# Kernel tuning notes

Hardware: AMD Instinct MI355X
Metric: run time of the kernel (lower is better)

Reference implementation:

```python
import jax, jax.numpy as jnp
import numpy as np

N, E = 20000, 320000
IN_F, EF, H, C = 2, 1, 128, 2
BN_S = 1.0 / float(np.sqrt(1.0 + 1e-5))  # eval-mode BatchNorm1d with running mean 0, var 1


def _gated_gcn_conv(h, e, src, dst, p, act, residual):
    # DGL GatedGCNConv: e' = C e + D h_src + E h_dst;
    # h' = A h + sum_{in-edges} sigmoid(e') * B h_src / (sum sigmoid(e') + 1e-6)
    Aw, Ab, Bw, Bb, Cw, Cb, Dw, Db, Ew, Eb, bhg, bhb, beg, beb = p
    h_in, e_in = h, e
    Ah = h @ Aw + Ab
    Bh = h @ Bw + Bb
    Dh = h @ Dw + Db
    Eh = h @ Ew + Eb
    e2 = e @ Cw + Cb + Dh[src] + Eh[dst]          # [E, H]
    sig = jax.nn.sigmoid(e2)
    num = jax.ops.segment_sum(sig * Bh[src], dst, num_segments=N)  # [N, H]
    den = jax.ops.segment_sum(sig, dst, num_segments=N)            # [N, H]
    h2 = Ah + num / (den + 1e-6)
    # BatchNorm (eval): (x - 0)/sqrt(1 + eps) * gamma + beta
    h2 = bhg * (h2 * BN_S) + bhb
    e2 = beg * (e2 * BN_S) + beb
    h2, e2 = act(h2), act(e2)
    if residual:
        h2 = h2 + h_in
        e2 = e2 + e_in
    return h2, e2


def _forward(node_feats, edge_feats, src, dst, P):
    (a0_w, a0_b, b0_w, b0_b, c0_w, c0_b, d0_w, d0_b, e0_w, e0_b,
     bnh0_g, bnh0_b, bne0_g, bne0_b,
     aL_w, aL_b, bL_w, bL_b, cL_w, cL_b, dL_w, dL_b, eL_w, eL_b,
     bnhL_g, bnhL_b, bneL_g, bneL_b,
     mlp_w1, mlp_b1, mlp_w2, mlp_b2) = P
    h, e = node_feats, edge_feats
    # layer 0: elu inside conv, residual off (2->128, 1->128)
    p0 = (a0_w, a0_b, b0_w, b0_b, c0_w, c0_b, d0_w, d0_b, e0_w, e0_b,
          bnh0_g, bnh0_b, bne0_g, bne0_b)
    h, e = _gated_gcn_conv(h, e, src, dst, p0, jax.nn.elu, residual=False)
    h = jax.nn.leaky_relu(h)
    e = jax.nn.leaky_relu(e)
    # layers 1..2: leaky_relu inside conv, residual on (128->128)
    for l in range(2):
        pl = (aL_w[l], aL_b[l], bL_w[l], bL_b[l], cL_w[l], cL_b[l],
              dL_w[l], dL_b[l], eL_w[l], eL_b[l],
              bnhL_g[l], bnhL_b[l], bneL_g[l], bneL_b[l])
        h, e = _gated_gcn_conv(h, e, src, dst, pl, jax.nn.leaky_relu, residual=True)
        h = jax.nn.leaky_relu(h)
        e = jax.nn.leaky_relu(e)
    # edge classifier: gather endpoints, concat with edge feats, MLP
    edge_repr = jnp.concatenate([h[src], h[dst], e], axis=1)  # [E, 3H]
    hid = jax.nn.relu(edge_repr @ mlp_w1 + mlp_b1)
    return hid @ mlp_w2 + mlp_b2                               # [E, C]


PARAM_NAMES = ["a0_w", "a0_b", "b0_w", "b0_b", "c0_w", "c0_b", "d0_w", "d0_b",
               "e0_w", "e0_b", "bnh0_g", "bnh0_b", "bne0_g", "bne0_b",
               "aL_w", "aL_b", "bL_w", "bL_b", "cL_w", "cL_b", "dL_w", "dL_b",
               "eL_w", "eL_b", "bnhL_g", "bnhL_b", "bneL_g", "bneL_b",
               "mlp_w1", "mlp_b1", "mlp_w2", "mlp_b2"]


def setup_inputs() -> dict:
    key = jax.random.key(0)
    ks = iter(jax.random.split(key, 64))
    nrm = lambda shp: jax.random.normal(next(ks), shp, dtype=jnp.float32) * 0.05
    inp = {}
    inp["node_feats"] = jax.random.normal(next(ks), (N, IN_F), dtype=jnp.float32)
    inp["edge_feats"] = jax.random.normal(next(ks), (E, EF), dtype=jnp.float32)
    inp["src"] = jax.random.randint(next(ks), (E,), 0, N, dtype=jnp.int32)
    inp["dst"] = jax.random.randint(next(ks), (E,), 0, N, dtype=jnp.int32)
    # layer 0 linears (A,B,D,E: in->H; C: edge->H), biases zero-init like common practice
    for nm, din in [("a0", IN_F), ("b0", IN_F), ("c0", EF), ("d0", IN_F), ("e0", IN_F)]:
        inp[nm + "_w"] = nrm((din, H))
        inp[nm + "_b"] = nrm((H,))
    inp["bnh0_g"] = jnp.ones((H,), jnp.float32)
    inp["bnh0_b"] = jnp.zeros((H,), jnp.float32)
    inp["bne0_g"] = jnp.ones((H,), jnp.float32)
    inp["bne0_b"] = jnp.zeros((H,), jnp.float32)
    # layers 1..2 stacked
    for nm in ["aL", "bL", "cL", "dL", "eL"]:
        inp[nm + "_w"] = nrm((2, H, H))
        inp[nm + "_b"] = nrm((2, H))
    inp["bnhL_g"] = jnp.ones((2, H), jnp.float32)
    inp["bnhL_b"] = jnp.zeros((2, H), jnp.float32)
    inp["bneL_g"] = jnp.ones((2, H), jnp.float32)
    inp["bneL_b"] = jnp.zeros((2, H), jnp.float32)
    # edge MLP
    inp["mlp_w1"] = nrm((3 * H, H))
    inp["mlp_b1"] = nrm((H,))
    inp["mlp_w2"] = nrm((H, C))
    inp["mlp_b2"] = nrm((C,))
    return inp


def reference(node_feats, edge_feats, src, dst,
              a0_w, a0_b, b0_w, b0_b, c0_w, c0_b, d0_w, d0_b, e0_w, e0_b,
              bnh0_g, bnh0_b, bne0_g, bne0_b,
              aL_w, aL_b, bL_w, bL_b, cL_w, cL_b, dL_w, dL_b, eL_w, eL_b,
              bnhL_g, bnhL_b, bneL_g, bneL_b,
              mlp_w1, mlp_b1, mlp_w2, mlp_b2):
    P = (a0_w, a0_b, b0_w, b0_b, c0_w, c0_b, d0_w, d0_b, e0_w, e0_b,
         bnh0_g, bnh0_b, bne0_g, bne0_b,
         aL_w, aL_b, bL_w, bL_b, cL_w, cL_b, dL_w, dL_b, eL_w, eL_b,
         bnhL_g, bnhL_b, bneL_g, bneL_b,
         mlp_w1, mlp_b1, mlp_w2, mlp_b2)
    return _forward(node_feats, edge_feats, src, dst, P)
```

## Files before the change

### kernel.cpp

```cpp
#include <hip/hip_runtime.h>
#include <hip/hip_bf16.h>
#include <math.h>

#define NN 20000
#define NE 320000
#define H 128
#define NH (NN * H)

typedef short bf16x8 __attribute__((ext_vector_type(8)));
typedef float f32x4 __attribute__((ext_vector_type(4)));
typedef unsigned short u16x8 __attribute__((ext_vector_type(8)));

__device__ __forceinline__ float lrelu(float x) { return x > 0.f ? x : 0.01f * x; }
__device__ __forceinline__ float eluf(float x)  { return x > 0.f ? x : expm1f(x); }
__device__ __forceinline__ float sigf(float x)  { return 1.f / (1.f + __expf(-x)); }
__device__ __forceinline__ unsigned short f2b(float x) {
    __hip_bfloat16 h = __float2bfloat16(x);
    return *reinterpret_cast<unsigned short*>(&h);
}
__device__ __forceinline__ float b2f(unsigned short u) {
    __hip_bfloat16 h = *reinterpret_cast<__hip_bfloat16*>(&u);
    return __bfloat162float(h);
}
#define BN_S 0.99999500003749973f

struct PackPtrs { const float* w[13]; };
__global__ __launch_bounds__(256) void k_pack(PackPtrs p, unsigned short* __restrict__ dst) {
    int gid = blockIdx.x * 256 + threadIdx.x;
    int m = gid >> 11;
    int r = gid & 2047;
    int t = r >> 8, kk = (r >> 6) & 3, lane = r & 63;
    const float* W = p.w[m];
    int col = t * 16 + (lane & 15);
    int krow = kk * 32 + (lane >> 4) * 8;
    unsigned short* o = dst + (size_t)m * 16384 + (size_t)r * 8;
#pragma unroll
    for (int j = 0; j < 8; ++j) o[j] = f2b(W[(krow + j) * H + col]);
}

__global__ __launch_bounds__(256) void k_deg(const int* __restrict__ dst, int* __restrict__ deg) {
    int e = blockIdx.x * 256 + threadIdx.x;
    if (e < NE) atomicAdd(&deg[dst[e]], 1);
}

__global__ __launch_bounds__(256) void k_scan(const int* __restrict__ deg,
                                              int* __restrict__ off, int* __restrict__ cursor) {
    __shared__ int sums[256];
    const int t = threadIdx.x;
    const int per = (NN + 255) / 256;
    const int base = t * per;
    int s = 0;
    for (int i = 0; i < per; ++i) { int idx = base + i; if (idx < NN) s += deg[idx]; }
    sums[t] = s;
    __syncthreads();
    for (int d = 1; d < 256; d <<= 1) {
        int v = (t >= d) ? sums[t - d] : 0;
        __syncthreads();
        sums[t] += v;
        __syncthreads();
    }
    int run = (t == 0) ? 0 : sums[t - 1];
    for (int i = 0; i < per; ++i) {
        int idx = base + i;
        if (idx < NN) { off[idx] = run; cursor[idx] = run; run += deg[idx]; }
    }
}

__global__ __launch_bounds__(256) void k_fill(const int* __restrict__ dst,
                                              int* __restrict__ cursor, int* __restrict__ csr) {
    int e = blockIdx.x * 256 + threadIdx.x;
    if (e < NE) {
        int pos = atomicAdd(&cursor[dst[e]], 1);
        csr[pos] = e;
    }
}

__global__ __launch_bounds__(256) void k_seqs(const int* __restrict__ csr,
                                              const int* __restrict__ src,
                                              const int* __restrict__ dst,
                                              const float* __restrict__ ef,
                                              int* __restrict__ srcseq,
                                              int* __restrict__ dstseq,
                                              float* __restrict__ efseq) {
    int pos = blockIdx.x * 256 + threadIdx.x;
    if (pos < NE) {
        int eid = csr[pos];
        srcseq[pos] = src[eid];
        dstseq[pos] = dst[eid];
        efseq[pos]  = ef[eid];
    }
}

__global__ __launch_bounds__(256) void k_nodelin0(
        const float* __restrict__ nf,
        const float* __restrict__ wa, const float* __restrict__ ba,
        const float* __restrict__ wb, const float* __restrict__ bb,
        const float* __restrict__ wd, const float* __restrict__ bd,
        const float* __restrict__ we, const float* __restrict__ be,
        float* __restrict__ lin0, unsigned short* __restrict__ linB,
        unsigned short* __restrict__ linD, unsigned short* __restrict__ linE) {
    int idx = blockIdx.x * 256 + threadIdx.x;
    int n = idx >> 7, c = idx & 127;
    float x0 = nf[n * 2], x1 = nf[n * 2 + 1];
    lin0[idx] = fmaf(x0, wa[c], fmaf(x1, wa[128 + c], ba[c]));
    linB[idx] = f2b(fmaf(x0, wb[c], fmaf(x1, wb[128 + c], bb[c])));
    linD[idx] = f2b(fmaf(x0, wd[c], fmaf(x1, wd[128 + c], bd[c])));
    linE[idx] = f2b(fmaf(x0, we[c], fmaf(x1, we[128 + c], be[c])));
}

__global__ __launch_bounds__(256) void k_edge0(
        const float* __restrict__ efseq,
        const float* __restrict__ cw, const float* __restrict__ cb,
        const int* __restrict__ srcseq, const int* __restrict__ dstseq,
        const unsigned short* __restrict__ linD, const unsigned short* __restrict__ linE,
        const float* __restrict__ g, const float* __restrict__ bt,
        unsigned short* __restrict__ ebuf) {
    const int tid = threadIdx.x;
    const int pos = blockIdx.x * 8 + (tid >> 5);
    const int c0 = (tid & 31) * 4;
    const int s = srcseq[pos], d = dstseq[pos];
    const float ev = efseq[pos];
    const float4 cw4 = *(const float4*)(cw + c0);
    const float4 cb4 = *(const float4*)(cb + c0);
    const ushort4 Dh = *(const ushort4*)(linD + (size_t)s * H + c0);
    const ushort4 Eh = *(const ushort4*)(linE + (size_t)d * H + c0);
    const float4 g4  = *(const float4*)(g + c0);
    const float4 bt4 = *(const float4*)(bt + c0);
    float e2[4] = { fmaf(ev, cw4.x, cb4.x) + b2f(Dh.x) + b2f(Eh.x),
                    fmaf(ev, cw4.y, cb4.y) + b2f(Dh.y) + b2f(Eh.y),
                    fmaf(ev, cw4.z, cb4.z) + b2f(Dh.z) + b2f(Eh.z),
                    fmaf(ev, cw4.w, cb4.w) + b2f(Dh.w) + b2f(Eh.w) };
    const float gg[4] = { g4.x, g4.y, g4.z, g4.w };
    const float bb[4] = { bt4.x, bt4.y, bt4.z, bt4.w };
    ushort4 u;
    u.x = f2b(lrelu(eluf(fmaf(gg[0], e2[0] * BN_S, bb[0]))));
    u.y = f2b(lrelu(eluf(fmaf(gg[1], e2[1] * BN_S, bb[1]))));
    u.z = f2b(lrelu(eluf(fmaf(gg[2], e2[2] * BN_S, bb[2]))));
    u.w = f2b(lrelu(eluf(fmaf(gg[3], e2[3] * BN_S, bb[3]))));
    *(ushort4*)(ebuf + (size_t)pos * H + c0) = u;
}

__global__ __launch_bounds__(256) void k_agg0(
        const int* __restrict__ off, const int* __restrict__ deg,
        const int* __restrict__ srcseq, const float* __restrict__ efseq,
        const float* __restrict__ cw, const float* __restrict__ cb,
        const float* __restrict__ lin0, const unsigned short* __restrict__ linB,
        const unsigned short* __restrict__ linD, const unsigned short* __restrict__ linE,
        const float* __restrict__ g, const float* __restrict__ bt,
        float* __restrict__ hout, unsigned short* __restrict__ hbout) {
    const int tid = threadIdx.x;
    const int n = blockIdx.x * 2 + (tid >> 7);
    const int c = tid & 127;
    const int base = off[n], dg = deg[n];
    float num = 0.f, den = 0.f;
    const float Ehn = b2f(linE[(size_t)n * H + c]);
    const float cwc = cw[c], cbc = cb[c];
    int i = 0;
    for (; i + 4 <= dg; i += 4) {
        int s0 = srcseq[base + i],     s1 = srcseq[base + i + 1];
        int s2 = srcseq[base + i + 2], s3 = srcseq[base + i + 3];
        float x0 = fmaf(efseq[base + i],     cwc, cbc) + b2f(linD[(size_t)s0 * H + c]) + Ehn;
        float x1 = fmaf(efseq[base + i + 1], cwc, cbc) + b2f(linD[(size_t)s1 * H + c]) + Ehn;
        float x2 = fmaf(efseq[base + i + 2], cwc, cbc) + b2f(linD[(size_t)s2 * H + c]) + Ehn;
        float x3 = fmaf(efseq[base + i + 3], cwc, cbc) + b2f(linD[(size_t)s3 * H + c]) + Ehn;
        float g0 = sigf(x0), g1 = sigf(x1), g2 = sigf(x2), g3 = sigf(x3);
        num = fmaf(g0, b2f(linB[(size_t)s0 * H + c]), num); den += g0;
        num = fmaf(g1, b2f(linB[(size_t)s1 * H + c]), num); den += g1;
        num = fmaf(g2, b2f(linB[(size_t)s2 * H + c]), num); den += g2;
        num = fmaf(g3, b2f(linB[(size_t)s3 * H + c]), num); den += g3;
    }
    for (; i < dg; ++i) {
        int sa = srcseq[base + i];
        float xa = fmaf(efseq[base + i], cwc, cbc) + b2f(linD[(size_t)sa * H + c]) + Ehn;
        float ga = sigf(xa);
        num = fmaf(ga, b2f(linB[(size_t)sa * H + c]), num); den += ga;
    }
    float h2 = lin0[(size_t)n * H + c] + num / (den + 1e-6f);
    h2 = fmaf(g[c], h2 * BN_S, bt[c]);
    h2 = eluf(h2);
    float r = lrelu(h2);
    hout[(size_t)n * H + c] = r;
    hbout[(size_t)n * H + c] = f2b(r);
}

__global__ __launch_bounds__(256) void k_agg(
        const int* __restrict__ off, const int* __restrict__ deg,
        const int* __restrict__ srcseq,
        const unsigned short* __restrict__ e2seq,
        const float* __restrict__ lin0, const unsigned short* __restrict__ linB,
        const float* __restrict__ g, const float* __restrict__ bt,
        const float* __restrict__ hin, float* __restrict__ hout,
        unsigned short* __restrict__ hbout) {
    const int tid = threadIdx.x;
    const int n = blockIdx.x * 2 + (tid >> 7);
    const int c = tid & 127;
    const int base = off[n], dg = deg[n];
    float num = 0.f, den = 0.f;
    int i = 0;
    for (; i + 4 <= dg; i += 4) {
        int s0 = srcseq[base + i],     s1 = srcseq[base + i + 1];
        int s2 = srcseq[base + i + 2], s3 = srcseq[base + i + 3];
        float x0 = b2f(e2seq[(size_t)(base + i) * H + c]);
        float x1 = b2f(e2seq[(size_t)(base + i + 1) * H + c]);
        float x2 = b2f(e2seq[(size_t)(base + i + 2) * H + c]);
        float x3 = b2f(e2seq[(size_t)(base + i + 3) * H + c]);
        float g0 = sigf(x0), g1 = sigf(x1), g2 = sigf(x2), g3 = sigf(x3);
        num = fmaf(g0, b2f(linB[(size_t)s0 * H + c]), num); den += g0;
        num = fmaf(g1, b2f(linB[(size_t)s1 * H + c]), num); den += g1;
        num = fmaf(g2, b2f(linB[(size_t)s2 * H + c]), num); den += g2;
        num = fmaf(g3, b2f(linB[(size_t)s3 * H + c]), num); den += g3;
    }
    for (; i < dg; ++i) {
        int sa = srcseq[base + i];
        float xa = b2f(e2seq[(size_t)(base + i) * H + c]);
        float ga = sigf(xa);
        num = fmaf(ga, b2f(linB[(size_t)sa * H + c]), num); den += ga;
    }
    float h2 = lin0[(size_t)n * H + c] + num / (den + 1e-6f);
    h2 = fmaf(g[c], h2 * BN_S, bt[c]);
    h2 = lrelu(h2);
    h2 += hin[(size_t)n * H + c];
    float r = lrelu(h2);
    hout[(size_t)n * H + c] = r;
    hbout[(size_t)n * H + c] = f2b(r);
}

__global__ __launch_bounds__(256) void k_nodegemm(
        const unsigned short* __restrict__ hb,
        const unsigned short* __restrict__ wpack,
        const float* __restrict__ ba, const float* __restrict__ bb,
        const float* __restrict__ bd, const float* __restrict__ be,
        float* __restrict__ lin0, unsigned short* __restrict__ linB,
        unsigned short* __restrict__ linD, unsigned short* __restrict__ linE) {
    __shared__ __align__(16) unsigned short AT[64][136];
    const int tid = threadIdx.x;
    const int nbase = blockIdx.x * 64;
    const int which = blockIdx.y;
    const unsigned short* Wp = wpack + (size_t)which * 16384;
    const float* B = which == 0 ? ba : which == 1 ? bb : which == 2 ? bd : be;
#pragma unroll
    for (int rep = 0; rep < 4; ++rep) {
        int flat = (rep * 256 + tid) * 8;
        int r = flat >> 7, k0 = flat & 127;
        int n = nbase + r;
        u16x8 v = {};
        if (n < NN) v = *(const u16x8*)(hb + (size_t)n * H + k0);
        *(u16x8*)(&AT[r][k0]) = v;
    }
    __syncthreads();
    const int lane = tid & 63, wave = tid >> 6;
    const int lrow = lane & 15, quad = lane >> 4;
    f32x4 acc[8] = {};
#pragma unroll
    for (int kk = 0; kk < 4; ++kk) {
        bf16x8 af = *(const bf16x8*)(&AT[wave * 16 + lrow][kk * 32 + quad * 8]);
#pragma unroll
        for (int t = 0; t < 8; ++t) {
            bf16x8 bfv = *(const bf16x8*)(Wp + ((t * 4 + kk) * 64 + lane) * 8);
            acc[t] = __builtin_amdgcn_mfma_f32_16x16x32_bf16(af, bfv, acc[t], 0, 0, 0);
        }
    }
    unsigned short* linX = which == 1 ? linB : which == 2 ? linD : linE;
#pragma unroll
    for (int t = 0; t < 8; ++t) {
        int col = t * 16 + lrow;
        float bv = B[col];
#pragma unroll
        for (int reg = 0; reg < 4; ++reg) {
            int n = nbase + wave * 16 + quad * 4 + reg;
            if (n < NN) {
                float v = acc[t][reg] + bv;
                if (which == 0) lin0[(size_t)n * H + col] = v;
                else            linX[(size_t)n * H + col] = f2b(v);
            }
        }
    }
}

__global__ __launch_bounds__(256) void k_pgemm(
        const unsigned short* __restrict__ hb,
        const unsigned short* __restrict__ w1p,
        const float* __restrict__ b1,
        unsigned short* __restrict__ P) {
    __shared__ __align__(16) unsigned short AT[64][136];
    const int tid = threadIdx.x;
    const int nbase = blockIdx.x * 64;
    const int y = blockIdx.y;
    const unsigned short* Wp = w1p + (size_t)y * 16384;
#pragma unroll
    for (int rep = 0; rep < 4; ++rep) {
        int flat = (rep * 256 + tid) * 8;
        int r = flat >> 7, k0 = flat & 127;
        int n = nbase + r;
        u16x8 v = {};
        if (n < NN) v = *(const u16x8*)(hb + (size_t)n * H + k0);
        *(u16x8*)(&AT[r][k0]) = v;
    }
    __syncthreads();
    const int lane = tid & 63, wave = tid >> 6;
    const int lrow = lane & 15, quad = lane >> 4;
    f32x4 acc[8] = {};
#pragma unroll
    for (int kk = 0; kk < 4; ++kk) {
        bf16x8 af = *(const bf16x8*)(&AT[wave * 16 + lrow][kk * 32 + quad * 8]);
#pragma unroll
        for (int t = 0; t < 8; ++t) {
            bf16x8 bfv = *(const bf16x8*)(Wp + ((t * 4 + kk) * 64 + lane) * 8);
            acc[t] = __builtin_amdgcn_mfma_f32_16x16x32_bf16(af, bfv, acc[t], 0, 0, 0);
        }
    }
#pragma unroll
    for (int t = 0; t < 8; ++t) {
        int col = t * 16 + lrow;
        float bv = (y == 0) ? b1[col] : 0.f;
#pragma unroll
        for (int reg = 0; reg < 4; ++reg) {
            int n = nbase + wave * 16 + quad * 4 + reg;
            if (n < NN)
                P[(size_t)y * NH + (size_t)n * H + col] = f2b(acc[t][reg] + bv);
        }
    }
}

__global__ __launch_bounds__(256) void k_edgegemm(
        unsigned short* __restrict__ ebuf,
        unsigned short* __restrict__ e2seq,
        const unsigned short* __restrict__ Wp,
        const float* __restrict__ cb,
        const int* __restrict__ srcseq, const int* __restrict__ dstseq,
        const unsigned short* __restrict__ linD,
        const unsigned short* __restrict__ linE,
        const float* __restrict__ g, const float* __restrict__ bt) {
    __shared__ __align__(16) unsigned short AT[64][136];
    const int tid = threadIdx.x;
    const int ebase = blockIdx.x * 64;
#pragma unroll
    for (int rep = 0; rep < 4; ++rep) {
        int flat = (rep * 256 + tid) * 8;
        int r = flat >> 7, k0 = flat & 127;
        *(u16x8*)(&AT[r][k0]) = *(const u16x8*)(ebuf + (size_t)(ebase + r) * H + k0);
    }
    __syncthreads();
    const int lane = tid & 63, wave = tid >> 6;
    const int lrow = lane & 15, quad = lane >> 4;
    f32x4 acc[8] = {};
#pragma unroll
    for (int kk = 0; kk < 4; ++kk) {
        bf16x8 af = *(const bf16x8*)(&AT[wave * 16 + lrow][kk * 32 + quad * 8]);
#pragma unroll
        for (int t = 0; t < 8; ++t) {
            bf16x8 bfv = *(const bf16x8*)(Wp + ((t * 4 + kk) * 64 + lane) * 8);
            acc[t] = __builtin_amdgcn_mfma_f32_16x16x32_bf16(af, bfv, acc[t], 0, 0, 0);
        }
    }
    const int r0 = ebase + wave * 16 + quad * 4;
    const int rr0 = wave * 16 + quad * 4;
    int sv[4], dv[4];
#pragma unroll
    for (int reg = 0; reg < 4; ++reg) {
        sv[reg] = srcseq[r0 + reg];
        dv[reg] = dstseq[r0 + reg];
    }
#pragma unroll
    for (int t = 0; t < 8; ++t) {
        int col = t * 16 + lrow;
        float cbv = cb[col], gv = g[col], btv = bt[col];
#pragma unroll
        for (int reg = 0; reg < 4; ++reg) {
            float Dh = b2f(linD[(size_t)sv[reg] * H + col]);
            float Eh = b2f(linE[(size_t)dv[reg] * H + col]);
            float e2 = acc[t][reg] + cbv + Dh + Eh;
            e2seq[(size_t)(r0 + reg) * H + col] = f2b(e2);
            float tt = lrelu(fmaf(gv, e2 * BN_S, btv));
            float ein = b2f(AT[rr0 + reg][col]);
            ebuf[(size_t)(r0 + reg) * H + col] = f2b(lrelu(tt + ein));
        }
    }
}

__global__ __launch_bounds__(256) void k_mlp2(
        const unsigned short* __restrict__ ebuf,
        const unsigned short* __restrict__ P,
        const int* __restrict__ csr,
        const int* __restrict__ srcseq, const int* __restrict__ dstseq,
        const unsigned short* __restrict__ w1p2,
        const float* __restrict__ w2, const float* __restrict__ b2,
        float* __restrict__ out) {
    __shared__ __align__(16) unsigned short AT[64][136];
    const int tid = threadIdx.x;
    const int ebase = blockIdx.x * 64;
#pragma unroll
    for (int rep = 0; rep < 4; ++rep) {
        int flat = (rep * 256 + tid) * 8;
        int r = flat >> 7, k0 = flat & 127;
        *(u16x8*)(&AT[r][k0]) = *(const u16x8*)(ebuf + (size_t)(ebase + r) * H + k0);
    }
    __syncthreads();
    const int lane = tid & 63, wave = tid >> 6;
    const int lrow = lane & 15, quad = lane >> 4;
    f32x4 acc[8] = {};
#pragma unroll
    for (int kk = 0; kk < 4; ++kk) {
        bf16x8 af = *(const bf16x8*)(&AT[wave * 16 + lrow][kk * 32 + quad * 8]);
#pragma unroll
        for (int t = 0; t < 8; ++t) {
            bf16x8 bfv = *(const bf16x8*)(w1p2 + ((t * 4 + kk) * 64 + lane) * 8);
            acc[t] = __builtin_amdgcn_mfma_f32_16x16x32_bf16(af, bfv, acc[t], 0, 0, 0);
        }
    }
    const int e0 = ebase + wave * 16 + quad * 4;
    const float b20 = b2[0], b21 = b2[1];
#pragma unroll
    for (int reg = 0; reg < 4; ++reg) {
        const int e = e0 + reg;
        const int s = srcseq[e], d = dstseq[e];
        float p1v[8], p2v[8];
#pragma unroll
        for (int t = 0; t < 8; ++t) {
            int col = t * 16 + lrow;
            p1v[t] = b2f(P[(size_t)s * H + col]);
            p2v[t] = b2f(P[(size_t)NH + (size_t)d * H + col]);
        }
        float p0 = 0.f, p1 = 0.f;
#pragma unroll
        for (int t = 0; t < 8; ++t) {
            int col = t * 16 + lrow;
            float hv = fmaxf(acc[t][reg] + p1v[t] + p2v[t], 0.f);
            p0 = fmaf(hv, w2[col * 2], p0);
            p1 = fmaf(hv, w2[col * 2 + 1], p1);
        }
#pragma unroll
        for (int off = 8; off; off >>= 1) {
            p0 += __shfl_xor(p0, off, 16);
            p1 += __shfl_xor(p1, off, 16);
        }
        if (lrow == 0) {
            int eid = csr[e];
            out[eid * 2]     = p0 + b20;
            out[eid * 2 + 1] = p1 + b21;
        }
    }
}

extern "C" void kernel_launch(void* const* d_in, const int* in_sizes, int n_in,
                              void* d_out, int out_size, void* d_ws, size_t ws_size,
                              hipStream_t stream) {
    const float* nf  = (const float*)d_in[0];
    const float* ef  = (const float*)d_in[1];
    const int*   src = (const int*)d_in[2];
    const int*   dst = (const int*)d_in[3];
    const float *a0w = (const float*)d_in[4],  *a0b = (const float*)d_in[5];
    const float *b0w = (const float*)d_in[6],  *b0b = (const float*)d_in[7];
    const float *c0w = (const float*)d_in[8],  *c0b = (const float*)d_in[9];
    const float *d0w = (const float*)d_in[10], *d0b = (const float*)d_in[11];
    const float *e0w = (const float*)d_in[12], *e0b = (const float*)d_in[13];
    const float *bnh0g = (const float*)d_in[14], *bnh0b = (const float*)d_in[15];
    const float *bne0g = (const float*)d_in[16], *bne0b = (const float*)d_in[17];
    const float *aLw = (const float*)d_in[18], *aLb = (const float*)d_in[19];
    const float *bLw = (const float*)d_in[20], *bLb = (const float*)d_in[21];
    const float *cLw = (const float*)d_in[22], *cLb = (const float*)d_in[23];
    const float *dLw = (const float*)d_in[24], *dLb = (const float*)d_in[25];
    const float *eLw = (const float*)d_in[26], *eLb = (const float*)d_in[27];
    const float *bnhLg = (const float*)d_in[28], *bnhLb = (const float*)d_in[29];
    const float *bneLg = (const float*)d_in[30], *bneLb = (const float*)d_in[31];
    const float *w1 = (const float*)d_in[32], *b1 = (const float*)d_in[33];
    const float *w2 = (const float*)d_in[34], *b2 = (const float*)d_in[35];
    float* out = (float*)d_out;

    char* ws = (char*)d_ws;
    unsigned short* ebuf  = (unsigned short*)ws;
    unsigned short* e2seq = ebuf + (size_t)NE * H;
    float* lin0 = (float*)(e2seq + (size_t)NE * H);
    unsigned short* linB = (unsigned short*)(lin0 + NH);
    unsigned short* linD = linB + NH;
    unsigned short* linE = linD + NH;
    float* h0  = (float*)(linE + NH);
    float* h1  = h0 + NH;
    unsigned short* hb0 = (unsigned short*)(h1 + NH);
    unsigned short* hb1 = hb0 + NH;
    int* deg    = (int*)(hb1 + NH);
    int* off    = deg + NN;
    int* cursor = off + NN;
    int* csr    = cursor + NN;
    int* srcseq = csr + NE;
    int* dstseq = srcseq + NE;
    float* efseq = (float*)(dstseq + NE);
    unsigned short* wpack = (unsigned short*)(efseq + NE);
    unsigned short* P = e2seq;

    PackPtrs pp;
    const size_t HH = (size_t)H * H;
    for (int l = 0; l < 2; ++l) {
        pp.w[l * 5 + 0] = aLw + l * HH;
        pp.w[l * 5 + 1] = bLw + l * HH;
        pp.w[l * 5 + 2] = dLw + l * HH;
        pp.w[l * 5 + 3] = eLw + l * HH;
        pp.w[l * 5 + 4] = cLw + l * HH;
    }
    pp.w[10] = w1; pp.w[11] = w1 + HH; pp.w[12] = w1 + 2 * HH;
    k_pack<<<104, 256, 0, stream>>>(pp, wpack);

    hipMemsetAsync(deg, 0, NN * sizeof(int), stream);
    k_deg<<<(NE + 255) / 256, 256, 0, stream>>>(dst, deg);
    k_scan<<<1, 256, 0, stream>>>(deg, off, cursor);
    k_fill<<<(NE + 255) / 256, 256, 0, stream>>>(dst, cursor, csr);
    k_seqs<<<(NE + 255) / 256, 256, 0, stream>>>(csr, src, dst, ef, srcseq, dstseq, efseq);

    k_nodelin0<<<NN * H / 256, 256, 0, stream>>>(nf, a0w, a0b, b0w, b0b, d0w, d0b,
                                                 e0w, e0b, lin0, linB, linD, linE);
    k_edge0<<<NE / 8, 256, 0, stream>>>(efseq, c0w, c0b, srcseq, dstseq, linD, linE,
                                        bne0g, bne0b, ebuf);
    k_agg0<<<NN / 2, 256, 0, stream>>>(off, deg, srcseq, efseq, c0w, c0b,
                                       lin0, linB, linD, linE, bnh0g, bnh0b, h0, hb0);

    for (int l = 0; l < 2; ++l) {
        const float* hin = (l == 0) ? h0 : h1;
        float* hout      = (l == 0) ? h1 : h0;
        const unsigned short* hbin = (l == 0) ? hb0 : hb1;
        unsigned short* hbout      = (l == 0) ? hb1 : hb0;
        k_nodegemm<<<dim3(313, 4), 256, 0, stream>>>(hbin,
            wpack + (size_t)l * 5 * 16384,
            aLb + l * H, bLb + l * H, dLb + l * H, eLb + l * H,
            lin0, linB, linD, linE);
        k_edgegemm<<<NE / 64, 256, 0, stream>>>(ebuf, e2seq,
                                                wpack + (size_t)(l * 5 + 4) * 16384,
                                                cLb + l * H, srcseq, dstseq,
                                                linD, linE,
                                                bneLg + l * H, bneLb + l * H);
        k_agg<<<NN / 2, 256, 0, stream>>>(off, deg, srcseq, e2seq,
                                          lin0, linB, bnhLg + l * H, bnhLb + l * H,
                                          hin, hout, hbout);
    }

    k_pgemm<<<dim3(313, 2), 256, 0, stream>>>(hb0, wpack + 10ull * 16384, b1, P);
    k_mlp2<<<NE / 64, 256, 0, stream>>>(ebuf, P, csr, srcseq, dstseq,
                                        wpack + 12ull * 16384, w2, b2, out);

    (void)in_sizes; (void)n_in; (void)out_size; (void)ws_size;
}
```

Measured before the change: 637.4 us.

## Fuse CSR fill with sequence gather, widen agg unroll, stage edge outputs through LDS

Merges k_seqs into k_fill so the permuted src/dst/edge-feature arrays are written at the same moment the atomic position is obtained, which removes one launch and one pass over csr. Raises the aggregation loop unroll from 4 to 8 so more gathers are in flight per thread. In the edge GEMM epilogue, the scattered 2-byte stores of ebuf and e2seq are replaced by writes into the shared tile, then 16-byte coalesced copies out to global memory. This costs extra __syncthreads, 32 more registers per thread for the staged e2 values, and some added register pressure from the wider unroll.

```diff
diff --git a/kernel.cpp b/kernel.cpp
--- a/kernel.cpp
+++ b/kernel.cpp
@@ -66,28 +66,20 @@
     }
 }
 
-__global__ __launch_bounds__(256) void k_fill(const int* __restrict__ dst,
-                                              int* __restrict__ cursor, int* __restrict__ csr) {
+__global__ __launch_bounds__(256) void k_fill(
+        const int* __restrict__ src, const int* __restrict__ dst,
+        const float* __restrict__ ef,
+        int* __restrict__ cursor, int* __restrict__ csr,
+        int* __restrict__ srcseq, int* __restrict__ dstseq,
+        float* __restrict__ efseq) {
     int e = blockIdx.x * 256 + threadIdx.x;
     if (e < NE) {
-        int pos = atomicAdd(&cursor[dst[e]], 1);
-        csr[pos] = e;
-    }
-}
-
-__global__ __launch_bounds__(256) void k_seqs(const int* __restrict__ csr,
-                                              const int* __restrict__ src,
-                                              const int* __restrict__ dst,
-                                              const float* __restrict__ ef,
-                                              int* __restrict__ srcseq,
-                                              int* __restrict__ dstseq,
-                                              float* __restrict__ efseq) {
-    int pos = blockIdx.x * 256 + threadIdx.x;
-    if (pos < NE) {
-        int eid = csr[pos];
-        srcseq[pos] = src[eid];
-        dstseq[pos] = dst[eid];
-        efseq[pos]  = ef[eid];
+        int d = dst[e];
+        int pos = atomicAdd(&cursor[d], 1);
+        csr[pos]    = e;
+        srcseq[pos] = src[e];
+        dstseq[pos] = d;
+        efseq[pos]  = ef[e];
     }
 }
 
@@ -197,18 +189,22 @@
     const int base = off[n], dg = deg[n];
     float num = 0.f, den = 0.f;
     int i = 0;
-    for (; i + 4 <= dg; i += 4) {
-        int s0 = srcseq[base + i],     s1 = srcseq[base + i + 1];
-        int s2 = srcseq[base + i + 2], s3 = srcseq[base + i + 3];
-        float x0 = b2f(e2seq[(size_t)(base + i) * H + c]);
-        float x1 = b2f(e2seq[(size_t)(base + i + 1) * H + c]);
-        float x2 = b2f(e2seq[(size_t)(base + i + 2) * H + c]);
-        float x3 = b2f(e2seq[(size_t)(base + i + 3) * H + c]);
-        float g0 = sigf(x0), g1 = sigf(x1), g2 = sigf(x2), g3 = sigf(x3);
-        num = fmaf(g0, b2f(linB[(size_t)s0 * H + c]), num); den += g0;
-        num = fmaf(g1, b2f(linB[(size_t)s1 * H + c]), num); den += g1;
-        num = fmaf(g2, b2f(linB[(size_t)s2 * H + c]), num); den += g2;
-        num = fmaf(g3, b2f(linB[(size_t)s3 * H + c]), num); den += g3;
+    for (; i + 8 <= dg; i += 8) {
+        int s[8];
+        float x[8];
+#pragma unroll
+        for (int j = 0; j < 8; ++j) {
+            s[j] = srcseq[base + i + j];
+            x[j] = b2f(e2seq[(size_t)(base + i + j) * H + c]);
+        }
+        float gg[8];
+#pragma unroll
+        for (int j = 0; j < 8; ++j) gg[j] = sigf(x[j]);
+#pragma unroll
+        for (int j = 0; j < 8; ++j) {
+            num = fmaf(gg[j], b2f(linB[(size_t)s[j] * H + c]), num);
+            den += gg[j];
+        }
     }
     for (; i < dg; ++i) {
         int sa = srcseq[base + i];
@@ -353,14 +349,14 @@
             acc[t] = __builtin_amdgcn_mfma_f32_16x16x32_bf16(af, bfv, acc[t], 0, 0, 0);
         }
     }
-    const int r0 = ebase + wave * 16 + quad * 4;
     const int rr0 = wave * 16 + quad * 4;
     int sv[4], dv[4];
 #pragma unroll
     for (int reg = 0; reg < 4; ++reg) {
-        sv[reg] = srcseq[r0 + reg];
-        dv[reg] = dstseq[r0 + reg];
-    }
+        sv[reg] = srcseq[ebase + rr0 + reg];
+        dv[reg] = dstseq[ebase + rr0 + reg];
+    }
+    unsigned short e2s[32];
 #pragma unroll
     for (int t = 0; t < 8; ++t) {
         int col = t * 16 + lrow;
@@ -370,11 +366,31 @@
             float Dh = b2f(linD[(size_t)sv[reg] * H + col]);
             float Eh = b2f(linE[(size_t)dv[reg] * H + col]);
             float e2 = acc[t][reg] + cbv + Dh + Eh;
-            e2seq[(size_t)(r0 + reg) * H + col] = f2b(e2);
+            e2s[t * 4 + reg] = f2b(e2);
             float tt = lrelu(fmaf(gv, e2 * BN_S, btv));
             float ein = b2f(AT[rr0 + reg][col]);
-            ebuf[(size_t)(r0 + reg) * H + col] = f2b(lrelu(tt + ein));
-        }
+            AT[rr0 + reg][col] = f2b(lrelu(tt + ein));
+        }
+    }
+    __syncthreads();
+#pragma unroll
+    for (int rep = 0; rep < 4; ++rep) {
+        int flat = (rep * 256 + tid) * 8;
+        int r = flat >> 7, k0 = flat & 127;
+        *(u16x8*)(ebuf + (size_t)(ebase + r) * H + k0) = *(const u16x8*)(&AT[r][k0]);
+    }
+    __syncthreads();
+#pragma unroll
+    for (int t = 0; t < 8; ++t)
+#pragma unroll
+        for (int reg = 0; reg < 4; ++reg)
+            AT[rr0 + reg][t * 16 + lrow] = e2s[t * 4 + reg];
+    __syncthreads();
+#pragma unroll
+    for (int rep = 0; rep < 4; ++rep) {
+        int flat = (rep * 256 + tid) * 8;
+        int r = flat >> 7, k0 = flat & 127;
+        *(u16x8*)(e2seq + (size_t)(ebase + r) * H + k0) = *(const u16x8*)(&AT[r][k0]);
     }
 }
 
@@ -503,8 +519,8 @@
     hipMemsetAsync(deg, 0, NN * sizeof(int), stream);
     k_deg<<<(NE + 255) / 256, 256, 0, stream>>>(dst, deg);
     k_scan<<<1, 256, 0, stream>>>(deg, off, cursor);
-    k_fill<<<(NE + 255) / 256, 256, 0, stream>>>(dst, cursor, csr);
-    k_seqs<<<(NE + 255) / 256, 256, 0, stream>>>(csr, src, dst, ef, srcseq, dstseq, efseq);
+    k_fill<<<(NE + 255) / 256, 256, 0, stream>>>(src, dst, ef, cursor, csr,
+                                                 srcseq, dstseq, efseq);
 
     k_nodelin0<<<NN * H / 256, 256, 0, stream>>>(nf, a0w, a0b, b0w, b0b, d0w, d0b,
                                                  e0w, e0b, lin0, linB, linD, linE);
```

Result: faster. 618.6 us, median of 2 (-3.0%).
